# Performance work log

Measured on AMD Instinct MI355X. Metric: run time of the kernel, lower is better.

## Reference

```python
import jax, jax.numpy as jnp
import numpy as np
import math

B, N, DMODEL, H = 8, 1024, 256, 8
HEAD_DIM = DMODEL // H


def setup_inputs() -> dict:
    key = jax.random.key(0)
    ks = jax.random.split(key, 8)
    x = jax.random.normal(ks[0], (B, N, DMODEL), dtype=jnp.float32)
    # symmetric-ish nonnegative pairwise distances
    adj = jax.random.uniform(ks[1], (B, N, N), dtype=jnp.float32) * 10.0
    mask = jax.random.uniform(ks[2], (B, N)) < 0.9  # bool, mostly valid nodes
    W_qkv = jax.random.normal(ks[3], (DMODEL, 3 * DMODEL), dtype=jnp.float32) / math.sqrt(DMODEL)
    b_qkv = jax.random.normal(ks[4], (3 * DMODEL,), dtype=jnp.float32) * 0.01
    shifts = jnp.arange(1.0, H + 1.0, dtype=jnp.float32)  # initial_shifts
    widths = jnp.ones((H,), dtype=jnp.float32)            # initial_widths
    # self_loop_W = 1/head_dim + U(0,1), non-trainable
    self_loop_w = 1.0 / HEAD_DIM + jax.random.uniform(ks[5], (H,), dtype=jnp.float32)
    return {"x": x, "adj": adj, "mask": mask, "W_qkv": W_qkv, "b_qkv": b_qkv,
            "shifts": shifts, "widths": widths, "self_loop_w": self_loop_w}


def reference(x, adj, mask, W_qkv, b_qkv, shifts, widths, self_loop_w):
    b, n, _ = x.shape
    h = shifts.shape[0]
    d = W_qkv.shape[1] // (3 * h)
    qkv = (x @ W_qkv + b_qkv).reshape(b, n, 3, h, d)
    qkv = jnp.transpose(qkv, (2, 0, 3, 1, 4))  # [3, B, H, N, D]
    Q, K, V = qkv[0], qkv[1], qkv[2]
    scores = jnp.einsum('bhnd,bhmd->bhnm', Q, K) / jnp.sqrt(jnp.float32(d))
    # Gaussian moire focus on adjacency distances, per head
    sh = shifts.reshape(1, h, 1, 1)
    w = jnp.maximum(widths, 0.5).reshape(1, h, 1, 1)
    moire = jnp.exp(-((adj[:, None, :, :] - sh) ** 2) / w)
    adjusted = scores + jnp.log(jnp.maximum(moire, 1e-6))
    eye = jnp.eye(n, dtype=adjusted.dtype)  # [N, N]
    adjusted = adjusted + eye * self_loop_w.reshape(1, h, 1, 1)
    mask2d = (mask[:, :, None] & mask[:, None, :])[:, None, :, :]  # [B,1,N,N]
    adjusted = jnp.where(mask2d, adjusted, jnp.float32(-1000000.0))
    attn = jax.nn.softmax(adjusted, axis=-1)
    out = jnp.einsum('bhnm,bhmd->bhnd', attn, V)
    return jnp.transpose(out, (0, 2, 1, 3)).reshape(b, n, h * d)
```

## Files before the change

kernel.cpp:

```cpp
#include <hip/hip_runtime.h>

#define BB 8
#define NN 1024
#define DM 256
#define HH 8
#define HD 32
#define TC 768

typedef __bf16 bf16x8 __attribute__((ext_vector_type(8)));
typedef __bf16 bf16x4 __attribute__((ext_vector_type(4)));
typedef __bf16 bf16x2 __attribute__((ext_vector_type(2)));
typedef float  f32x4  __attribute__((ext_vector_type(4)));
typedef int    i32x4  __attribute__((ext_vector_type(4)));
typedef unsigned int u32;

__global__ __launch_bounds__(256) void precast(
    const float* __restrict__ x, const float* __restrict__ W,
    __bf16* __restrict__ xb, __bf16* __restrict__ Wt)
{
  const int tid = threadIdx.x;
  const int bid = blockIdx.x;
  if (bid < 48) {
    __shared__ __bf16 T[64][65];
    const int ct = bid % 12, kt = bid / 12;
    const int c0 = ct * 64, k0 = kt * 64;
    #pragma unroll
    for (int i = 0; i < 16; ++i) {
      int e = tid + i * 256, kk = e >> 6, cc = e & 63;
      T[cc][kk] = (__bf16)W[(size_t)(k0 + kk) * TC + c0 + cc];
    }
    __syncthreads();
    #pragma unroll
    for (int i = 0; i < 16; ++i) {
      int e = tid + i * 256, cc = e >> 6, kk = e & 63;
      Wt[(size_t)(c0 + cc) * DM + k0 + kk] = T[cc][kk];
    }
  } else {
    const size_t e = (size_t)(bid - 48) * 256 + tid;
    const float4 v = ((const float4*)x)[e];
    bf16x4 o;
    o[0] = (__bf16)v.x; o[1] = (__bf16)v.y;
    o[2] = (__bf16)v.z; o[3] = (__bf16)v.w;
    ((bf16x4*)xb)[e] = o;
  }
}

__global__ __launch_bounds__(256, 3) void qkv_gemm(
    const __bf16* __restrict__ xb, const __bf16* __restrict__ Wt,
    const float* __restrict__ bias, __bf16* __restrict__ Qb,
    __bf16* __restrict__ Kb, __bf16* __restrict__ Vt)
{
  __shared__ __align__(16) char LDSU[49152];
  __bf16* As0 = (__bf16*)LDSU;
  __bf16* Bs0 = (__bf16*)(LDSU + 16384);
  __bf16* As1 = (__bf16*)(LDSU + 24576);
  __bf16* Bs1 = (__bf16*)(LDSU + 40960);

  const int tid  = threadIdx.x;
  const int w    = tid >> 6, lane = tid & 63;
  const int n16  = lane & 15, quad = lane >> 4;
  const int m0   = blockIdx.y * 128, c0 = blockIdx.x * 64;
  const int bb   = m0 >> 10, n0 = m0 & 1023;

  const int stRow = w*8 + (lane >> 3);
  const int stG   = (lane & 7) ^ (lane >> 3);
  const __bf16* gA = &xb[(size_t)(m0 + stRow)*DM + stG*8];
  const __bf16* gB = &Wt[(size_t)(c0 + stRow)*DM + stG*8];

#define QKV_STAGE(Adst, Bdst, K0) do {                                        \
    _Pragma("unroll")                                                         \
    for (int i_ = 0; i_ < 4; ++i_) {                                          \
      const __bf16* gp_ = gA + (size_t)(i_*32)*DM + (K0);                     \
      __bf16* lp_ = (Adst) + (i_*32 + w*8)*64;                                \
      __builtin_amdgcn_global_load_lds(                                       \
          (const __attribute__((address_space(1))) u32*)gp_,                  \
          (__attribute__((address_space(3))) u32*)lp_, 16, 0, 0);             \
    }                                                                         \
    _Pragma("unroll")                                                         \
    for (int i_ = 0; i_ < 2; ++i_) {                                          \
      const __bf16* gp_ = gB + (size_t)(i_*32)*DM + (K0);                     \
      __bf16* lp_ = (Bdst) + (i_*32 + w*8)*64;                                \
      __builtin_amdgcn_global_load_lds(                                       \
          (const __attribute__((address_space(1))) u32*)gp_,                  \
          (__attribute__((address_space(3))) u32*)lp_, 16, 0, 0);             \
    }                                                                         \
  } while (0)

  f32x4 acc[2][4] = {};

  QKV_STAGE(As0, Bs0, 0);
  __syncthreads();

  #pragma unroll
  for (int kk = 0; kk < 4; ++kk) {
    __bf16* Ac = (kk & 1) ? As1 : As0;
    __bf16* Bc = (kk & 1) ? Bs1 : Bs0;
    if (kk == 0)      QKV_STAGE(As1, Bs1, 64);
    else if (kk == 1) QKV_STAGE(As0, Bs0, 128);
    else if (kk == 2) QKV_STAGE(As1, Bs1, 192);
    #pragma unroll
    for (int ks = 0; ks < 2; ++ks) {
      const int ch = ((ks*4 + quad) ^ (n16 & 7)) * 8;
      bf16x8 af0 = *(const bf16x8*)&Ac[(w*32 + n16)*64 + ch];
      bf16x8 af1 = *(const bf16x8*)&Ac[(w*32 + 16 + n16)*64 + ch];
      #pragma unroll
      for (int cb = 0; cb < 4; ++cb) {
        bf16x8 bfb = *(const bf16x8*)&Bc[(cb*16 + n16)*64 + ch];
        acc[0][cb] = __builtin_amdgcn_mfma_f32_16x16x32_bf16(af0, bfb, acc[0][cb], 0, 0, 0);
        acc[1][cb] = __builtin_amdgcn_mfma_f32_16x16x32_bf16(af1, bfb, acc[1][cb], 0, 0, 0);
      }
    }
    __syncthreads();
  }

  float bv[4];
  #pragma unroll
  for (int cb = 0; cb < 4; ++cb) bv[cb] = bias[c0 + cb*16 + n16];

  if (c0 < 512) {
    __bf16* Ct = (__bf16*)LDSU;
    #pragma unroll
    for (int cb = 0; cb < 4; ++cb)
      #pragma unroll
      for (int mb = 0; mb < 2; ++mb)
        #pragma unroll
        for (int r = 0; r < 4; ++r)
          Ct[(w*32 + mb*16 + quad*4 + r)*72 + cb*16 + n16] =
              (__bf16)(acc[mb][cb][r] + bv[cb]);
    __syncthreads();
    const int chunk = tid & 3, hh = (tid >> 2) & 1, rbase = tid >> 3;
    const int c_head = c0 + hh*32;
    const int h = (c_head >> 5) & 7;
    __bf16* base = (c_head >> 8) ? Kb : Qb;
    #pragma unroll
    for (int it = 0; it < 4; ++it) {
      int rl = rbase + it*32;
      bf16x8 v = *(const bf16x8*)&Ct[rl*72 + hh*32 + chunk*8];
      *(bf16x8*)&base[((size_t)((bb*HH + h)*NN + n0 + rl))*HD + chunk*8] = v;
    }
  } else {
    __bf16* CtT = (__bf16*)LDSU;
    #pragma unroll
    for (int cb = 0; cb < 4; ++cb)
      #pragma unroll
      for (int mb = 0; mb < 2; ++mb) {
        bf16x4 t;
        #pragma unroll
        for (int r = 0; r < 4; ++r) t[r] = (__bf16)(acc[mb][cb][r] + bv[cb]);
        *(bf16x4*)&CtT[(cb*16 + n16)*136 + w*32 + mb*16 + quad*4] = t;
      }
    __syncthreads();
    const int col = tid >> 2, sg = tid & 3;
    const int c = c0 + col;
    const int h = (c >> 5) & 7, dd = c & 31;
    __bf16* dst = &Vt[((size_t)((bb*HH + h)*HD + dd))*NN + n0 + sg*32];
    const __bf16* srcp = &CtT[col*136 + sg*32];
    #pragma unroll
    for (int q2 = 0; q2 < 4; ++q2)
      *(bf16x8*)&dst[q2*8] = *(const bf16x8*)&srcp[q2*8];
  }
}

__global__ __launch_bounds__(256, 4) void attn_kernel(
    const __bf16* __restrict__ Q, const __bf16* __restrict__ K,
    const __bf16* __restrict__ Vt, const float* __restrict__ adj,
    const int* __restrict__ mask, const float* __restrict__ shifts,
    const float* __restrict__ widths, const float* __restrict__ slw,
    float* __restrict__ out)
{
  __shared__ __align__(16) char PsU[8192];
  __shared__ __align__(16) __bf16 Ks[2][64][40];
  __shared__ __align__(16) __bf16 Vts[2][32][72];

  const int tid  = threadIdx.x;
  const int w    = tid >> 6, lane = tid & 63;
  const int n16  = lane & 15, quad = lane >> 4;
  const int bh   = blockIdx.x >> 4, qt = blockIdx.x & 15;
  const int b    = bh >> 3, h = bh & 7;
  const int q0   = qt * 64;

  const float L2E   = 1.4426950408889634f;
  const float sh    = shifts[h];
  const float ninvw = -L2E / fmaxf(widths[h], 0.5f);
  const float slv   = slw[h] * L2E;
  const float scl   = 0.17677669529663687f * L2E;
  const float MASKV = -28.0f;
  const float c1 = -2.0f * sh * ninvw;
  const float c2 = sh * sh * ninvw;

  const int srow = tid >> 2, sseg = tid & 3;
  const int vd   = tid >> 3, vsg  = tid & 7;

  const __bf16* Kg = K + (size_t)bh*NN*HD;
  const __bf16* Vg = Vt + (size_t)bh*HD*NN;

  const bf16x8 qf =
      *(const bf16x8*)&Q[((size_t)bh*NN + q0 + w*16 + n16)*HD + quad*8];

  {
    *(bf16x8*)&Ks[0][srow][sseg*8] = *(const bf16x8*)&Kg[srow*HD + sseg*8];
    *(bf16x8*)&Vts[0][vd][vsg*8]   = *(const bf16x8*)&Vg[(size_t)vd*NN + vsg*8];
  }

  const bool mqv = mask[b*NN + q0 + w*16 + n16] != 0;

  const float* aq  = adj + ((size_t)(b*NN + q0 + w*16 + n16))*NN + quad*4;
  const int*   mjp = mask + b*NN + quad*4;

  f32x4 av[2][4];
  #pragma unroll
  for (int cb = 0; cb < 4; ++cb) av[0][cb] = *(const f32x4*)&aq[cb*16];

  char* PsRow = PsU + (w*16 + n16)*128;
  const int swzM  = (n16 & 7) * 16;
  const int swzW  = (quad*8) ^ swzM;
  const int swzR0 = (quad*16) ^ swzM;
  const int swzR1 = (64 + quad*16) ^ swzM;
  const int dloc  = w*16 + n16 - quad*4;

  const f32x4 zero = {0.f, 0.f, 0.f, 0.f};
  f32x4 o0 = zero, o1 = zero, lacc = zero;
  bf16x8 onesb;
  #pragma unroll
  for (int i = 0; i < 8; ++i) onesb[i] = (__bf16)1.0f;

  __syncthreads();

  #pragma unroll 2
  for (int jtl = 0; jtl < 16; ++jtl) {
    const int cur = jtl & 1, nxt = cur ^ 1;
    const int j0  = jtl * 64;

    bf16x8 kn, vn;
    if (jtl < 15) {
      kn = *(const bf16x8*)&Kg[(j0 + 64 + srow)*HD + sseg*8];
      vn = *(const bf16x8*)&Vg[(size_t)vd*NN + j0 + 64 + vsg*8];
      #pragma unroll
      for (int cb = 0; cb < 4; ++cb)
        av[nxt][cb] = *(const f32x4*)&aq[j0 + 64 + cb*16];
    }

    i32x4 mj[4];
    #pragma unroll
    for (int cb = 0; cb < 4; ++cb) mj[cb] = *(const i32x4*)&mjp[j0 + cb*16];

    f32x4 s[4];
    #pragma unroll
    for (int cb = 0; cb < 4; ++cb) {
      bf16x8 kf = *(const bf16x8*)&Ks[cur][cb*16 + n16][quad*8];
      s[cb] = __builtin_amdgcn_mfma_f32_16x16x32_bf16(kf, qf, zero, 0, 0, 0);
    }

    const bool diagtile = (jtl == qt);
    #pragma unroll
    for (int cb = 0; cb < 4; ++cb) {
      float p[4];
      #pragma unroll
      for (int r = 0; r < 4; ++r) {
        float a   = av[cur][cb][r];
        float mo  = fmaf(a, fmaf(a, ninvw, c1), c2);
        float val = fmaf(s[cb][r], scl, mo);
        if (diagtile && (cb*16 + r == dloc)) val += slv;
        bool ok = mqv && (mj[cb][r] != 0);
        val = ok ? val : MASKV;
        p[r] = __builtin_amdgcn_exp2f(val);
      }
      bf16x2 w0, w1;
      w0[0] = (__bf16)p[0]; w0[1] = (__bf16)p[1];
      w1[0] = (__bf16)p[2]; w1[1] = (__bf16)p[3];
      *(bf16x2*)(PsRow + ((cb*32 + 0) ^ swzW)) = w0;
      *(bf16x2*)(PsRow + ((cb*32 + 4) ^ swzW)) = w1;
    }

    bf16x8 a0  = *(const bf16x8*)(PsRow + swzR0);
    bf16x8 a1  = *(const bf16x8*)(PsRow + swzR1);
    bf16x8 b00 = *(const bf16x8*)&Vts[cur][n16][quad*8];
    bf16x8 b01 = *(const bf16x8*)&Vts[cur][n16][32 + quad*8];
    bf16x8 b10 = *(const bf16x8*)&Vts[cur][16 + n16][quad*8];
    bf16x8 b11 = *(const bf16x8*)&Vts[cur][16 + n16][32 + quad*8];
    o0   = __builtin_amdgcn_mfma_f32_16x16x32_bf16(a0, b00, o0, 0, 0, 0);
    o0   = __builtin_amdgcn_mfma_f32_16x16x32_bf16(a1, b01, o0, 0, 0, 0);
    o1   = __builtin_amdgcn_mfma_f32_16x16x32_bf16(a0, b10, o1, 0, 0, 0);
    o1   = __builtin_amdgcn_mfma_f32_16x16x32_bf16(a1, b11, o1, 0, 0, 0);
    lacc = __builtin_amdgcn_mfma_f32_16x16x32_bf16(a0, onesb, lacc, 0, 0, 0);
    lacc = __builtin_amdgcn_mfma_f32_16x16x32_bf16(a1, onesb, lacc, 0, 0, 0);

    if (jtl < 15) {
      *(bf16x8*)&Ks[nxt][srow][sseg*8] = kn;
      *(bf16x8*)&Vts[nxt][vd][vsg*8]   = vn;
    }
    __syncthreads();
  }

  #pragma unroll
  for (int r = 0; r < 4; ++r) {
    const float invl = 1.0f / lacc[r];
    const int n = q0 + w*16 + quad*4 + r;
    float* og = out + ((size_t)(b*NN + n))*DM + h*HD;
    og[n16]      = o0[r] * invl;
    og[16 + n16] = o1[r] * invl;
  }
}

extern "C" void kernel_launch(void* const* d_in, const int* in_sizes, int n_in,
                              void* d_out, int out_size, void* d_ws, size_t ws_size,
                              hipStream_t stream) {
  const float* x      = (const float*)d_in[0];
  const float* adj    = (const float*)d_in[1];
  const int*   mask   = (const int*)d_in[2];
  const float* W      = (const float*)d_in[3];
  const float* bias   = (const float*)d_in[4];
  const float* shifts = (const float*)d_in[5];
  const float* widths = (const float*)d_in[6];
  const float* slwp   = (const float*)d_in[7];
  float* out = (float*)d_out;

  const size_t BHND = (size_t)BB*HH*NN*HD;
  const size_t WTN  = (size_t)TC*DM;
  __bf16* xbuf = (__bf16*)d_ws;
  __bf16* Wt   = xbuf + BHND;
  __bf16* Qb   = Wt + WTN;
  __bf16* Kb   = Qb + BHND;
  __bf16* Vt   = Kb + BHND;

  precast<<<dim3(48 + (int)(BHND/4/256)), 256, 0, stream>>>(x, W, xbuf, Wt);
  qkv_gemm<<<dim3(TC/64, (BB*NN)/128), 256, 0, stream>>>(xbuf, Wt, bias, Qb, Kb, Vt);
  attn_kernel<<<dim3(BB*HH*16), 256, 0, stream>>>(Qb, Kb, Vt, adj, mask,
                                                  shifts, widths, slwp, out);
}
```

Baseline: 147.5 us.

## Transpose score MFMA orientation and reorder blocks head-major for adj reuse

The block index is remapped so consecutive blocks share a head across batches and query tiles rather than sharing (b,h). The QK MFMA operands are swapped so each lane holds four query rows at one key column. Adjacency is then read as scalar per-row loads coalesced across n16 instead of f32x4 per lane, and P is written to LDS as single bf16 stores through a new swizzle. The intent is to change the adj access pattern and L2 locality of this memory-bound kernel, at the cost of more, narrower loads and LDS stores.

```diff
diff --git a/kernel.cpp b/kernel.cpp
--- a/kernel.cpp
+++ b/kernel.cpp
@@ -9,9 +9,7 @@
 
 typedef __bf16 bf16x8 __attribute__((ext_vector_type(8)));
 typedef __bf16 bf16x4 __attribute__((ext_vector_type(4)));
-typedef __bf16 bf16x2 __attribute__((ext_vector_type(2)));
 typedef float  f32x4  __attribute__((ext_vector_type(4)));
-typedef int    i32x4  __attribute__((ext_vector_type(4)));
 typedef unsigned int u32;
 
 __global__ __launch_bounds__(256) void precast(
@@ -175,8 +173,10 @@
   const int tid  = threadIdx.x;
   const int w    = tid >> 6, lane = tid & 63;
   const int n16  = lane & 15, quad = lane >> 4;
-  const int bh   = blockIdx.x >> 4, qt = blockIdx.x & 15;
-  const int b    = bh >> 3, h = bh & 7;
+  const int h    = blockIdx.x >> 7;
+  const int lo   = blockIdx.x & 127;
+  const int b    = lo >> 4, qt = lo & 15;
+  const int bh   = b*8 + h;
   const int q0   = qt * 64;
 
   const float L2E   = 1.4426950408889634f;
@@ -201,22 +201,44 @@
     *(bf16x8*)&Ks[0][srow][sseg*8] = *(const bf16x8*)&Kg[srow*HD + sseg*8];
     *(bf16x8*)&Vts[0][vd][vsg*8]   = *(const bf16x8*)&Vg[(size_t)vd*NN + vsg*8];
   }
-
-  const bool mqv = mask[b*NN + q0 + w*16 + n16] != 0;
-
-  const float* aq  = adj + ((size_t)(b*NN + q0 + w*16 + n16))*NN + quad*4;
-  const int*   mjp = mask + b*NN + quad*4;
-
-  f32x4 av[2][4];
-  #pragma unroll
-  for (int cb = 0; cb < 4; ++cb) av[0][cb] = *(const f32x4*)&aq[cb*16];
-
-  char* PsRow = PsU + (w*16 + n16)*128;
-  const int swzM  = (n16 & 7) * 16;
-  const int swzW  = (quad*8) ^ swzM;
-  const int swzR0 = (quad*16) ^ swzM;
-  const int swzR1 = (64 + quad*16) ^ swzM;
-  const int dloc  = w*16 + n16 - quad*4;
+  int mq[4];
+  #pragma unroll
+  for (int r = 0; r < 4; ++r) mq[r] = mask[b*NN + q0 + w*16 + quad*4 + r];
+
+  const float* arow0 = adj + ((size_t)(b*NN + q0 + w*16 + quad*4))*NN + n16;
+  const float* arow1 = arow0 + NN;
+  const float* arow2 = arow0 + 2*NN;
+  const float* arow3 = arow0 + 3*NN;
+  const int*   mrp   = mask + b*NN + n16;
+
+  float av[2][4][4];
+  int   mj[2][4];
+  #pragma unroll
+  for (int cb = 0; cb < 4; ++cb) mj[0][cb] = mrp[cb*16];
+  #pragma unroll
+  for (int cb = 0; cb < 4; ++cb) {
+    av[0][0][cb] = arow0[cb*16];
+    av[0][1][cb] = arow1[cb*16];
+    av[0][2][cb] = arow2[cb*16];
+    av[0][3][cb] = arow3[cb*16];
+  }
+  arow0 += 64; arow1 += 64; arow2 += 64; arow3 += 64; mrp += 64;
+
+  const int w16q4 = w*16 + quad*4;
+  const int hi    = n16 >> 3;
+  const int lo2   = (n16 & 7) * 2;
+  const int S01   = (w16q4 >> 1) & 7;
+  const int S23   = ((w16q4 >> 1) + 1) & 7;
+  char* PsW01[4]; char* PsW23[4];
+  #pragma unroll
+  for (int cb = 0; cb < 4; ++cb) {
+    PsW01[cb] = PsU + (size_t)w16q4*128     + ((((2*cb + hi) ^ S01) << 4) + lo2);
+    PsW23[cb] = PsU + (size_t)(w16q4+2)*128 + ((((2*cb + hi) ^ S23) << 4) + lo2);
+  }
+  const int rowR = w*16 + n16;
+  const int SR   = (n16 >> 1) & 7;
+  const char* PsR0 = PsU + (size_t)rowR*128 + (((quad ^ SR)    ) << 4);
+  const char* PsR1 = PsU + (size_t)rowR*128 + (((quad ^ SR) ^ 4) << 4);
 
   const f32x4 zero = {0.f, 0.f, 0.f, 0.f};
   f32x4 o0 = zero, o1 = zero, lacc = zero;
@@ -236,44 +258,44 @@
       kn = *(const bf16x8*)&Kg[(j0 + 64 + srow)*HD + sseg*8];
       vn = *(const bf16x8*)&Vg[(size_t)vd*NN + j0 + 64 + vsg*8];
       #pragma unroll
-      for (int cb = 0; cb < 4; ++cb)
-        av[nxt][cb] = *(const f32x4*)&aq[j0 + 64 + cb*16];
-    }
-
-    i32x4 mj[4];
-    #pragma unroll
-    for (int cb = 0; cb < 4; ++cb) mj[cb] = *(const i32x4*)&mjp[j0 + cb*16];
+      for (int cb = 0; cb < 4; ++cb) mj[nxt][cb] = mrp[cb*16];
+      #pragma unroll
+      for (int cb = 0; cb < 4; ++cb) {
+        av[nxt][0][cb] = arow0[cb*16];
+        av[nxt][1][cb] = arow1[cb*16];
+        av[nxt][2][cb] = arow2[cb*16];
+        av[nxt][3][cb] = arow3[cb*16];
+      }
+      arow0 += 64; arow1 += 64; arow2 += 64; arow3 += 64; mrp += 64;
+    }
 
     f32x4 s[4];
     #pragma unroll
     for (int cb = 0; cb < 4; ++cb) {
       bf16x8 kf = *(const bf16x8*)&Ks[cur][cb*16 + n16][quad*8];
-      s[cb] = __builtin_amdgcn_mfma_f32_16x16x32_bf16(kf, qf, zero, 0, 0, 0);
+      s[cb] = __builtin_amdgcn_mfma_f32_16x16x32_bf16(qf, kf, zero, 0, 0, 0);
     }
 
     const bool diagtile = (jtl == qt);
     #pragma unroll
-    for (int cb = 0; cb < 4; ++cb) {
-      float p[4];
-      #pragma unroll
-      for (int r = 0; r < 4; ++r) {
-        float a   = av[cur][cb][r];
+    for (int r = 0; r < 4; ++r) {
+      const int rowl = w16q4 + r;
+      #pragma unroll
+      for (int cb = 0; cb < 4; ++cb) {
+        float a   = av[cur][r][cb];
         float mo  = fmaf(a, fmaf(a, ninvw, c1), c2);
         float val = fmaf(s[cb][r], scl, mo);
-        if (diagtile && (cb*16 + r == dloc)) val += slv;
-        bool ok = mqv && (mj[cb][r] != 0);
+        if (diagtile && (cb*16 + n16 == rowl)) val += slv;
+        bool ok = (mq[r] != 0) && (mj[cur][cb] != 0);
         val = ok ? val : MASKV;
-        p[r] = __builtin_amdgcn_exp2f(val);
+        float p = __builtin_amdgcn_exp2f(val);
+        char* wp = (r < 2 ? PsW01[cb] : PsW23[cb]) + (r & 1) * 128;
+        *(__bf16*)wp = (__bf16)p;
       }
-      bf16x2 w0, w1;
-      w0[0] = (__bf16)p[0]; w0[1] = (__bf16)p[1];
-      w1[0] = (__bf16)p[2]; w1[1] = (__bf16)p[3];
-      *(bf16x2*)(PsRow + ((cb*32 + 0) ^ swzW)) = w0;
-      *(bf16x2*)(PsRow + ((cb*32 + 4) ^ swzW)) = w1;
-    }
-
-    bf16x8 a0  = *(const bf16x8*)(PsRow + swzR0);
-    bf16x8 a1  = *(const bf16x8*)(PsRow + swzR1);
+    }
+
+    bf16x8 a0  = *(const bf16x8*)PsR0;
+    bf16x8 a1  = *(const bf16x8*)PsR1;
     bf16x8 b00 = *(const bf16x8*)&Vts[cur][n16][quad*8];
     bf16x8 b01 = *(const bf16x8*)&Vts[cur][n16][32 + quad*8];
     bf16x8 b10 = *(const bf16x8*)&Vts[cur][16 + n16][quad*8];
```

New measurement: 133.8 us. 9.3% less time.

## Permute K rows in shared memory so P stays in registers for PV MFMA

Applied to the files above, without the earlier changes.

K rows are stored in LDS under a permutation, so each lane's QK^T MFMA output lands in the key-column order the PV MFMA A-operand expects. The probabilities can then be packed straight into bf16x8 registers, removing the LDS scratch buffer, its swizzled writes and the read-back. Adjacency and mask loads are regrouped to match the new column mapping. This saves LDS traffic and 8KB of shared memory per block, but depends on the permutation being exactly right for correctness.

```diff
diff --git a/kernel.cpp b/kernel.cpp
--- a/kernel.cpp
+++ b/kernel.cpp
@@ -9,7 +9,6 @@
 
 typedef __bf16 bf16x8 __attribute__((ext_vector_type(8)));
 typedef __bf16 bf16x4 __attribute__((ext_vector_type(4)));
-typedef __bf16 bf16x2 __attribute__((ext_vector_type(2)));
 typedef float  f32x4  __attribute__((ext_vector_type(4)));
 typedef int    i32x4  __attribute__((ext_vector_type(4)));
 typedef unsigned int u32;
@@ -168,7 +167,6 @@
     const float* __restrict__ widths, const float* __restrict__ slw,
     float* __restrict__ out)
 {
-  __shared__ __align__(16) char PsU[8192];
   __shared__ __align__(16) __bf16 Ks[2][64][40];
   __shared__ __align__(16) __bf16 Vts[2][32][72];
 
@@ -189,6 +187,7 @@
   const float c2 = sh * sh * ninvw;
 
   const int srow = tid >> 2, sseg = tid & 3;
+  const int phiRow = (srow & 35) + (((srow >> 2) & 1) << 4) + (((srow >> 3) & 3) << 2);
   const int vd   = tid >> 3, vsg  = tid & 7;
 
   const __bf16* Kg = K + (size_t)bh*NN*HD;
@@ -198,25 +197,23 @@
       *(const bf16x8*)&Q[((size_t)bh*NN + q0 + w*16 + n16)*HD + quad*8];
 
   {
-    *(bf16x8*)&Ks[0][srow][sseg*8] = *(const bf16x8*)&Kg[srow*HD + sseg*8];
-    *(bf16x8*)&Vts[0][vd][vsg*8]   = *(const bf16x8*)&Vg[(size_t)vd*NN + vsg*8];
+    *(bf16x8*)&Ks[0][phiRow][sseg*8] = *(const bf16x8*)&Kg[srow*HD + sseg*8];
+    *(bf16x8*)&Vts[0][vd][vsg*8]     = *(const bf16x8*)&Vg[(size_t)vd*NN + vsg*8];
   }
 
   const bool mqv = mask[b*NN + q0 + w*16 + n16] != 0;
 
-  const float* aq  = adj + ((size_t)(b*NN + q0 + w*16 + n16))*NN + quad*4;
-  const int*   mjp = mask + b*NN + quad*4;
-
-  f32x4 av[2][4];
-  #pragma unroll
-  for (int cb = 0; cb < 4; ++cb) av[0][cb] = *(const f32x4*)&aq[cb*16];
-
-  char* PsRow = PsU + (w*16 + n16)*128;
-  const int swzM  = (n16 & 7) * 16;
-  const int swzW  = (quad*8) ^ swzM;
-  const int swzR0 = (quad*16) ^ swzM;
-  const int swzR1 = (64 + quad*16) ^ swzM;
-  const int dloc  = w*16 + n16 - quad*4;
+  const float* aqp = adj + ((size_t)(b*NN + q0 + w*16 + n16))*NN + 8*quad;
+  const int*   mjp = mask + b*NN + 8*quad;
+
+  f32x4 av[2][2][2];
+  #pragma unroll
+  for (int a = 0; a < 2; ++a)
+    #pragma unroll
+    for (int b2 = 0; b2 < 2; ++b2)
+      av[0][a][b2] = *(const f32x4*)&aqp[32*a + 4*b2];
+
+  const int dloc8 = w*16 + n16 - 8*quad;
 
   const f32x4 zero = {0.f, 0.f, 0.f, 0.f};
   f32x4 o0 = zero, o1 = zero, lacc = zero;
@@ -236,58 +233,61 @@
       kn = *(const bf16x8*)&Kg[(j0 + 64 + srow)*HD + sseg*8];
       vn = *(const bf16x8*)&Vg[(size_t)vd*NN + j0 + 64 + vsg*8];
       #pragma unroll
-      for (int cb = 0; cb < 4; ++cb)
-        av[nxt][cb] = *(const f32x4*)&aq[j0 + 64 + cb*16];
-    }
-
-    i32x4 mj[4];
-    #pragma unroll
-    for (int cb = 0; cb < 4; ++cb) mj[cb] = *(const i32x4*)&mjp[j0 + cb*16];
+      for (int a = 0; a < 2; ++a)
+        #pragma unroll
+        for (int b2 = 0; b2 < 2; ++b2)
+          av[nxt][a][b2] = *(const f32x4*)&aqp[j0 + 64 + 32*a + 4*b2];
+    }
+
+    i32x4 mj[2][2];
+    #pragma unroll
+    for (int a = 0; a < 2; ++a)
+      #pragma unroll
+      for (int b2 = 0; b2 < 2; ++b2)
+        mj[a][b2] = *(const i32x4*)&mjp[j0 + 32*a + 4*b2];
 
     f32x4 s[4];
     #pragma unroll
-    for (int cb = 0; cb < 4; ++cb) {
-      bf16x8 kf = *(const bf16x8*)&Ks[cur][cb*16 + n16][quad*8];
-      s[cb] = __builtin_amdgcn_mfma_f32_16x16x32_bf16(kf, qf, zero, 0, 0, 0);
+    for (int c = 0; c < 4; ++c) {
+      bf16x8 kf = *(const bf16x8*)&Ks[cur][c*16 + n16][quad*8];
+      s[c] = __builtin_amdgcn_mfma_f32_16x16x32_bf16(kf, qf, zero, 0, 0, 0);
     }
 
     const bool diagtile = (jtl == qt);
-    #pragma unroll
-    for (int cb = 0; cb < 4; ++cb) {
-      float p[4];
-      #pragma unroll
-      for (int r = 0; r < 4; ++r) {
-        float a   = av[cur][cb][r];
-        float mo  = fmaf(a, fmaf(a, ninvw, c1), c2);
-        float val = fmaf(s[cb][r], scl, mo);
-        if (diagtile && (cb*16 + r == dloc)) val += slv;
-        bool ok = mqv && (mj[cb][r] != 0);
-        val = ok ? val : MASKV;
-        p[r] = __builtin_amdgcn_exp2f(val);
+    bf16x8 pa0, pa1;
+    #pragma unroll
+    for (int a = 0; a < 2; ++a)
+      #pragma unroll
+      for (int b2 = 0; b2 < 2; ++b2) {
+        const int c = 2*a + b2;
+        #pragma unroll
+        for (int r = 0; r < 4; ++r) {
+          float ad  = av[cur][a][b2][r];
+          float mo  = fmaf(ad, fmaf(ad, ninvw, c1), c2);
+          float val = fmaf(s[c][r], scl, mo);
+          if (diagtile && (32*a + 4*b2 + r) == dloc8) val += slv;
+          bool ok = mqv && (mj[a][b2][r] != 0);
+          val = ok ? val : MASKV;
+          float p = __builtin_amdgcn_exp2f(val);
+          if (a == 0) pa0[4*b2 + r] = (__bf16)p;
+          else        pa1[4*b2 + r] = (__bf16)p;
+        }
       }
-      bf16x2 w0, w1;
-      w0[0] = (__bf16)p[0]; w0[1] = (__bf16)p[1];
-      w1[0] = (__bf16)p[2]; w1[1] = (__bf16)p[3];
-      *(bf16x2*)(PsRow + ((cb*32 + 0) ^ swzW)) = w0;
-      *(bf16x2*)(PsRow + ((cb*32 + 4) ^ swzW)) = w1;
-    }
-
-    bf16x8 a0  = *(const bf16x8*)(PsRow + swzR0);
-    bf16x8 a1  = *(const bf16x8*)(PsRow + swzR1);
+
     bf16x8 b00 = *(const bf16x8*)&Vts[cur][n16][quad*8];
     bf16x8 b01 = *(const bf16x8*)&Vts[cur][n16][32 + quad*8];
     bf16x8 b10 = *(const bf16x8*)&Vts[cur][16 + n16][quad*8];
     bf16x8 b11 = *(const bf16x8*)&Vts[cur][16 + n16][32 + quad*8];
-    o0   = __builtin_amdgcn_mfma_f32_16x16x32_bf16(a0, b00, o0, 0, 0, 0);
-    o0   = __builtin_amdgcn_mfma_f32_16x16x32_bf16(a1, b01, o0, 0, 0, 0);
-    o1   = __builtin_amdgcn_mfma_f32_16x16x32_bf16(a0, b10, o1, 0, 0, 0);
-    o1   = __builtin_amdgcn_mfma_f32_16x16x32_bf16(a1, b11, o1, 0, 0, 0);
-    lacc = __builtin_amdgcn_mfma_f32_16x16x32_bf16(a0, onesb, lacc, 0, 0, 0);
-    lacc = __builtin_amdgcn_mfma_f32_16x16x32_bf16(a1, onesb, lacc, 0, 0, 0);
+    o0   = __builtin_amdgcn_mfma_f32_16x16x32_bf16(pa0, b00, o0, 0, 0, 0);
+    o0   = __builtin_amdgcn_mfma_f32_16x16x32_bf16(pa1, b01, o0, 0, 0, 0);
+    o1   = __builtin_amdgcn_mfma_f32_16x16x32_bf16(pa0, b10, o1, 0, 0, 0);
+    o1   = __builtin_amdgcn_mfma_f32_16x16x32_bf16(pa1, b11, o1, 0, 0, 0);
+    lacc = __builtin_amdgcn_mfma_f32_16x16x32_bf16(pa0, onesb, lacc, 0, 0, 0);
+    lacc = __builtin_amdgcn_mfma_f32_16x16x32_bf16(pa1, onesb, lacc, 0, 0, 0);
 
     if (jtl < 15) {
-      *(bf16x8*)&Ks[nxt][srow][sseg*8] = kn;
-      *(bf16x8*)&Vts[nxt][vd][vsg*8]   = vn;
+      *(bf16x8*)&Ks[nxt][phiRow][sseg*8] = kn;
+      *(bf16x8*)&Vts[nxt][vd][vsg*8]     = vn;
     }
     __syncthreads();
   }
```

After: 147.9 us. Within noise of the previous version (+0.2%).

## Split attention key tiles across waves with async LDS loads and smaller query tiles

Applied to the files above, without the earlier changes.

The attention kernel now processes 32 query rows per block instead of 64, doubling the grid. The four waves are arranged as two query groups times two key halves, and each wave's partial output and row sums are combined through LDS at the end. K and V tiles are fetched with global_load_lds into XOR-swizzled, unpadded LDS buffers, replacing the register staging, and the occupancy hint is raised to 8 blocks. Probability tiles are now written one bf16 element at a time, and the adj register double-buffering is gone, which may expose more load latency and LDS traffic.

```diff
diff --git a/kernel.cpp b/kernel.cpp
--- a/kernel.cpp
+++ b/kernel.cpp
@@ -9,9 +9,7 @@
 
 typedef __bf16 bf16x8 __attribute__((ext_vector_type(8)));
 typedef __bf16 bf16x4 __attribute__((ext_vector_type(4)));
-typedef __bf16 bf16x2 __attribute__((ext_vector_type(2)));
 typedef float  f32x4  __attribute__((ext_vector_type(4)));
-typedef int    i32x4  __attribute__((ext_vector_type(4)));
 typedef unsigned int u32;
 
 __global__ __launch_bounds__(256) void precast(
@@ -161,23 +159,24 @@
   }
 }
 
-__global__ __launch_bounds__(256, 4) void attn_kernel(
+__global__ __launch_bounds__(256, 8) void attn_kernel(
     const __bf16* __restrict__ Q, const __bf16* __restrict__ K,
     const __bf16* __restrict__ Vt, const float* __restrict__ adj,
     const int* __restrict__ mask, const float* __restrict__ shifts,
     const float* __restrict__ widths, const float* __restrict__ slw,
     float* __restrict__ out)
 {
-  __shared__ __align__(16) char PsU[8192];
-  __shared__ __align__(16) __bf16 Ks[2][64][40];
-  __shared__ __align__(16) __bf16 Vts[2][32][72];
+  __shared__ __align__(16) __bf16 Ks[2][64][32];
+  __shared__ __align__(16) __bf16 Vts[2][32][64];
+  __shared__ __align__(16) __bf16 Ps[32][72];
 
   const int tid  = threadIdx.x;
   const int w    = tid >> 6, lane = tid & 63;
   const int n16  = lane & 15, quad = lane >> 4;
-  const int bh   = blockIdx.x >> 4, qt = blockIdx.x & 15;
+  const int qg   = w >> 1, jh = w & 1;
+  const int bh   = blockIdx.x >> 5, qt = blockIdx.x & 31;
   const int b    = bh >> 3, h = bh & 7;
-  const int q0   = qt * 64;
+  const int q0   = qt * 32;
 
   const float L2E   = 1.4426950408889634f;
   const float sh    = shifts[h];
@@ -190,33 +189,36 @@
 
   const int srow = tid >> 2, sseg = tid & 3;
   const int vd   = tid >> 3, vsg  = tid & 7;
-
   const __bf16* Kg = K + (size_t)bh*NN*HD;
   const __bf16* Vg = Vt + (size_t)bh*HD*NN;
+  const __bf16* ksrc = Kg + srow*HD + (sseg ^ (srow & 3))*8;
+  const __bf16* vsrc = Vg + (size_t)vd*NN + (vsg ^ (vd & 7))*8;
+  __bf16* kdst0 = &Ks[0][0][0] + tid*8;
+  __bf16* kdst1 = &Ks[1][0][0] + tid*8;
+  __bf16* vdst0 = &Vts[0][0][0] + tid*8;
+  __bf16* vdst1 = &Vts[1][0][0] + tid*8;
+
+#define GLDS(g, l) __builtin_amdgcn_global_load_lds(                          \
+    (const __attribute__((address_space(1))) u32*)(g),                        \
+    (__attribute__((address_space(3))) u32*)(l), 16, 0, 0)
+
+  GLDS(ksrc, kdst0);
+  GLDS(vsrc, vdst0);
 
   const bf16x8 qf =
-      *(const bf16x8*)&Q[((size_t)bh*NN + q0 + w*16 + n16)*HD + quad*8];
-
-  {
-    *(bf16x8*)&Ks[0][srow][sseg*8] = *(const bf16x8*)&Kg[srow*HD + sseg*8];
-    *(bf16x8*)&Vts[0][vd][vsg*8]   = *(const bf16x8*)&Vg[(size_t)vd*NN + vsg*8];
-  }
-
-  const bool mqv = mask[b*NN + q0 + w*16 + n16] != 0;
-
-  const float* aq  = adj + ((size_t)(b*NN + q0 + w*16 + n16))*NN + quad*4;
-  const int*   mjp = mask + b*NN + quad*4;
-
-  f32x4 av[2][4];
+      *(const bf16x8*)&Q[((size_t)bh*NN + q0 + qg*16 + n16)*HD + quad*8];
+  int mq[4];
   #pragma unroll
-  for (int cb = 0; cb < 4; ++cb) av[0][cb] = *(const f32x4*)&aq[cb*16];
-
-  char* PsRow = PsU + (w*16 + n16)*128;
-  const int swzM  = (n16 & 7) * 16;
-  const int swzW  = (quad*8) ^ swzM;
-  const int swzR0 = (quad*16) ^ swzM;
-  const int swzR1 = (64 + quad*16) ^ swzM;
-  const int dloc  = w*16 + n16 - quad*4;
+  for (int r = 0; r < 4; ++r) mq[r] = mask[b*NN + q0 + qg*16 + quad*4 + r];
+
+  const float* ar0 = adj + ((size_t)(b*NN + q0 + qg*16 + quad*4))*NN + jh*32 + n16;
+  const float* ar1 = ar0 + NN;
+  const float* ar2 = ar0 + 2*NN;
+  const float* ar3 = ar0 + 3*NN;
+  const int*   mrp = mask + b*NN + jh*32 + n16;
+
+  const int kbc = (quad ^ (n16 & 3)) * 8;
+  const int vbc = (((jh << 2) + quad) ^ (n16 & 7)) * 8;
 
   const f32x4 zero = {0.f, 0.f, 0.f, 0.f};
   f32x4 o0 = zero, o1 = zero, lacc = zero;
@@ -224,81 +226,88 @@
   #pragma unroll
   for (int i = 0; i < 8; ++i) onesb[i] = (__bf16)1.0f;
 
+  const bool mydiagH = (jh == (qt & 1));
+  const int  dT  = qt >> 1;
+  const int  dlr = n16 - quad*4;
+
   __syncthreads();
 
   #pragma unroll 2
   for (int jtl = 0; jtl < 16; ++jtl) {
-    const int cur = jtl & 1, nxt = cur ^ 1;
+    const int cur = jtl & 1;
     const int j0  = jtl * 64;
 
-    bf16x8 kn, vn;
     if (jtl < 15) {
-      kn = *(const bf16x8*)&Kg[(j0 + 64 + srow)*HD + sseg*8];
-      vn = *(const bf16x8*)&Vg[(size_t)vd*NN + j0 + 64 + vsg*8];
+      const __bf16* kg = ksrc + (size_t)(j0 + 64)*HD;
+      const __bf16* vg = vsrc + (j0 + 64);
+      if (cur) { GLDS(kg, kdst0); GLDS(vg, vdst0); }
+      else     { GLDS(kg, kdst1); GLDS(vg, vdst1); }
+    }
+
+    int mj[2];
+    #pragma unroll
+    for (int cb = 0; cb < 2; ++cb) mj[cb] = mrp[j0 + cb*16];
+    float av[4][2];
+    #pragma unroll
+    for (int cb = 0; cb < 2; ++cb) {
+      av[0][cb] = ar0[j0 + cb*16];
+      av[1][cb] = ar1[j0 + cb*16];
+      av[2][cb] = ar2[j0 + cb*16];
+      av[3][cb] = ar3[j0 + cb*16];
+    }
+
+    f32x4 s[2];
+    #pragma unroll
+    for (int cb = 0; cb < 2; ++cb) {
+      bf16x8 kf = *(const bf16x8*)&Ks[cur][jh*32 + cb*16 + n16][kbc];
+      s[cb] = __builtin_amdgcn_mfma_f32_16x16x32_bf16(qf, kf, zero, 0, 0, 0);
+    }
+    bf16x8 b0 = *(const bf16x8*)&Vts[cur][n16][vbc];
+    bf16x8 b1 = *(const bf16x8*)&Vts[cur][16 + n16][vbc];
+
+    const bool diagt = mydiagH && (jtl == dT);
+    #pragma unroll
+    for (int r = 0; r < 4; ++r) {
       #pragma unroll
-      for (int cb = 0; cb < 4; ++cb)
-        av[nxt][cb] = *(const f32x4*)&aq[j0 + 64 + cb*16];
-    }
-
-    i32x4 mj[4];
-    #pragma unroll
-    for (int cb = 0; cb < 4; ++cb) mj[cb] = *(const i32x4*)&mjp[j0 + cb*16];
-
-    f32x4 s[4];
-    #pragma unroll
-    for (int cb = 0; cb < 4; ++cb) {
-      bf16x8 kf = *(const bf16x8*)&Ks[cur][cb*16 + n16][quad*8];
-      s[cb] = __builtin_amdgcn_mfma_f32_16x16x32_bf16(kf, qf, zero, 0, 0, 0);
-    }
-
-    const bool diagtile = (jtl == qt);
-    #pragma unroll
-    for (int cb = 0; cb < 4; ++cb) {
-      float p[4];
-      #pragma unroll
-      for (int r = 0; r < 4; ++r) {
-        float a   = av[cur][cb][r];
+      for (int cb = 0; cb < 2; ++cb) {
+        float a   = av[r][cb];
         float mo  = fmaf(a, fmaf(a, ninvw, c1), c2);
         float val = fmaf(s[cb][r], scl, mo);
-        if (diagtile && (cb*16 + r == dloc)) val += slv;
-        bool ok = mqv && (mj[cb][r] != 0);
+        if (diagt && (cb == qg) && (dlr == r)) val += slv;
+        bool ok = (mq[r] != 0) && (mj[cb] != 0);
         val = ok ? val : MASKV;
-        p[r] = __builtin_amdgcn_exp2f(val);
+        Ps[qg*16 + quad*4 + r][jh*32 + cb*16 + n16] =
+            (__bf16)__builtin_amdgcn_exp2f(val);
       }
-      bf16x2 w0, w1;
-      w0[0] = (__bf16)p[0]; w0[1] = (__bf16)p[1];
-      w1[0] = (__bf16)p[2]; w1[1] = (__bf16)p[3];
-      *(bf16x2*)(PsRow + ((cb*32 + 0) ^ swzW)) = w0;
-      *(bf16x2*)(PsRow + ((cb*32 + 4) ^ swzW)) = w1;
-    }
-
-    bf16x8 a0  = *(const bf16x8*)(PsRow + swzR0);
-    bf16x8 a1  = *(const bf16x8*)(PsRow + swzR1);
-    bf16x8 b00 = *(const bf16x8*)&Vts[cur][n16][quad*8];
-    bf16x8 b01 = *(const bf16x8*)&Vts[cur][n16][32 + quad*8];
-    bf16x8 b10 = *(const bf16x8*)&Vts[cur][16 + n16][quad*8];
-    bf16x8 b11 = *(const bf16x8*)&Vts[cur][16 + n16][32 + quad*8];
-    o0   = __builtin_amdgcn_mfma_f32_16x16x32_bf16(a0, b00, o0, 0, 0, 0);
-    o0   = __builtin_amdgcn_mfma_f32_16x16x32_bf16(a1, b01, o0, 0, 0, 0);
-    o1   = __builtin_amdgcn_mfma_f32_16x16x32_bf16(a0, b10, o1, 0, 0, 0);
-    o1   = __builtin_amdgcn_mfma_f32_16x16x32_bf16(a1, b11, o1, 0, 0, 0);
+    }
+
+    bf16x8 a0 = *(const bf16x8*)&Ps[qg*16 + n16][jh*32 + quad*8];
+    o0   = __builtin_amdgcn_mfma_f32_16x16x32_bf16(a0, b0, o0, 0, 0, 0);
+    o1   = __builtin_amdgcn_mfma_f32_16x16x32_bf16(a0, b1, o1, 0, 0, 0);
     lacc = __builtin_amdgcn_mfma_f32_16x16x32_bf16(a0, onesb, lacc, 0, 0, 0);
-    lacc = __builtin_amdgcn_mfma_f32_16x16x32_bf16(a1, onesb, lacc, 0, 0, 0);
-
-    if (jtl < 15) {
-      *(bf16x8*)&Ks[nxt][srow][sseg*8] = kn;
-      *(bf16x8*)&Vts[nxt][vd][vsg*8]   = vn;
-    }
-    __syncthreads();
-  }
-
-  #pragma unroll
-  for (int r = 0; r < 4; ++r) {
-    const float invl = 1.0f / lacc[r];
-    const int n = q0 + w*16 + quad*4 + r;
-    float* og = out + ((size_t)(b*NN + n))*DM + h*HD;
-    og[n16]      = o0[r] * invl;
-    og[16 + n16] = o1[r] * invl;
+
+    __syncthreads();
+  }
+
+  float* red = (float*)&Ks[0][0][0];
+  if (jh) {
+    float* p = red + (size_t)(qg*64 + lane)*12;
+    *(f32x4*)&p[0] = o0; *(f32x4*)&p[4] = o1; *(f32x4*)&p[8] = lacc;
+  }
+  __syncthreads();
+  if (!jh) {
+    const float* p = red + (size_t)(qg*64 + lane)*12;
+    o0   += *(const f32x4*)&p[0];
+    o1   += *(const f32x4*)&p[4];
+    lacc += *(const f32x4*)&p[8];
+    #pragma unroll
+    for (int r = 0; r < 4; ++r) {
+      const float invl = 1.0f / lacc[r];
+      const int n = q0 + qg*16 + quad*4 + r;
+      float* og = out + ((size_t)(b*NN + n))*DM + h*HD;
+      og[n16]      = o0[r] * invl;
+      og[16 + n16] = o1[r] * invl;
+    }
   }
 }
 
@@ -325,6 +334,6 @@
 
   precast<<<dim3(48 + (int)(BHND/4/256)), 256, 0, stream>>>(x, W, xbuf, Wt);
   qkv_gemm<<<dim3(TC/64, (BB*NN)/128), 256, 0, stream>>>(xbuf, Wt, bias, Qb, Kb, Vt);
-  attn_kernel<<<dim3(BB*HH*16), 256, 0, stream>>>(Qb, Kb, Vt, adj, mask,
+  attn_kernel<<<dim3(BB*HH*32), 256, 0, stream>>>(Qb, Kb, Vt, adj, mask,
                                                   shifts, widths, slwp, out);
 }
```

Result: faster. 137.9 us (-6.5%).
